# Performance work log

Hardware: AMD Instinct MI355X
Metric: run time of the kernel (lower is better)

## Reference

```python
import jax, jax.numpy as jnp
import numpy as np

HID = 10
IN_DIM = 256
B, H, W = 8, 96, 96


def _conv(x, w, b=None, pad=0):
    y = jax.lax.conv_general_dilated(x, w, (1, 1), [(pad, pad), (pad, pad)],
                                     dimension_numbers=('NCHW', 'OIHW', 'NCHW'))
    return y if b is None else y + b[None, :, None, None]


def _bn(x, g, b):
    # eval-mode InPlaceABN(Sync) with identity running stats -> per-channel affine
    return x * g[None, :, None, None] + b[None, :, None, None]


def _branch(x, w1, g1, b1, w2, g2, b2):
    # Conv3x3 -> BN -> ReLU -> Conv1x1 -> BN -> ReLU  (relation / comp_u / comp_l)
    y = jax.nn.relu(_bn(_conv(x, w1, pad=1), g1, b1))
    return jax.nn.relu(_bn(_conv(y, w2), g2, b2))


def _gru(x, h, gw, gb, cw, cg, cb):
    # ConvGRU with 1x1 kernels
    gates = _conv(jnp.concatenate([x, h], axis=1), gw, gb)
    r = jax.nn.sigmoid(gates[:, 0:1])
    u = jax.nn.sigmoid(gates[:, 1:2])
    cnm = jax.nn.relu(_bn(_conv(jnp.concatenate([x, r * h], axis=1), cw), cg, cb))
    return (1.0 - u) * h + u * cnm


def setup_inputs():
    key = jax.random.key(0)
    ks = iter(jax.random.split(key, 48))

    def nrm(shape, s=0.05):
        return jax.random.normal(next(ks), shape, jnp.float32) * s

    inp = {
        'f_nodes': jax.random.normal(next(ks), (2, B, HID, H, W), jnp.float32),
        'h_nodes': jax.random.normal(next(ks), (3, B, HID, H, W), jnp.float32),
        'p_nodes': jax.random.normal(next(ks), (7, B, HID, H, W), jnp.float32),
        'xh': jax.random.normal(next(ks), (B, IN_DIM, H, W), jnp.float32),
        'f_atts': jax.random.uniform(next(ks), (2, B, 1, H, W), jnp.float32),
        'p_atts': jax.random.uniform(next(ks), (7, B, 1, H, W), jnp.float32),
        # Decomposition.decomp_att: Conv3x3(257->256)+BN+ReLU, Conv1x1(256->2)+bias
        'da_w1': nrm((IN_DIM, IN_DIM + 1, 3, 3)),
        'da_g1': jnp.ones((IN_DIM,), jnp.float32),
        'da_b1': jnp.zeros((IN_DIM,), jnp.float32),
        'da_w2': nrm((2, IN_DIM, 1, 1)),
        'da_b2': jnp.zeros((2,), jnp.float32),
    }
    # relation (shared across children), comp_u, comp_l: Conv3x3(20->10)+BN+ReLU, Conv1x1(10->10)+BN+ReLU
    for p in ('rel', 'cu', 'cl'):
        inp[p + '_w1'] = nrm((HID, 2 * HID, 3, 3))
        inp[p + '_g1'] = jnp.ones((HID,), jnp.float32)
        inp[p + '_b1'] = jnp.zeros((HID,), jnp.float32)
        inp[p + '_w2'] = nrm((HID, HID, 1, 1))
        inp[p + '_g2'] = jnp.ones((HID,), jnp.float32)
        inp[p + '_b2'] = jnp.zeros((HID,), jnp.float32)
    # 3 ConvGRUs (cls_h), 1x1 kernels, stacked on leading dim
    inp['gru_gw'] = nrm((3, 2, 2 * HID, 1, 1))
    inp['gru_gb'] = jnp.zeros((3, 2), jnp.float32)
    inp['gru_cw'] = nrm((3, HID, 2 * HID, 1, 1))
    inp['gru_cg'] = jnp.ones((3, HID), jnp.float32)
    inp['gru_cb'] = jnp.zeros((3, HID), jnp.float32)
    return inp


def reference(f_nodes, h_nodes, p_nodes, xh, f_atts, p_atts,
              da_w1, da_g1, da_b1, da_w2, da_b2,
              rel_w1, rel_g1, rel_b1, rel_w2, rel_g2, rel_b2,
              cu_w1, cu_g1, cu_b1, cu_w2, cu_g2, cu_b2,
              cl_w1, cl_g1, cl_b1, cl_w2, cl_g2, cl_b2,
              gru_gw, gru_gb, gru_cw, gru_cg, gru_cb):
    parent, parent_att = f_nodes[1], f_atts[1]
    # Decomposition of full-body node into 2 half nodes
    dm = _conv(jnp.concatenate([parent_att, xh], axis=1), da_w1, pad=1)
    dm = jax.nn.relu(_bn(dm, da_g1, da_b1))
    dm = _conv(dm, da_w2, da_b2)  # [B, 2, H, W] decomposition map
    datt = jax.nn.softmax(dm, axis=1)
    decomp = [_branch(jnp.concatenate([parent * datt[:, i:i + 1] * parent_att,
                                       h_nodes[1 + i]], axis=1),
                      rel_w1, rel_g1, rel_b1, rel_w2, rel_g2, rel_b2)
              for i in range(2)]
    # node 0: background
    n0 = _gru(f_nodes[0] + p_nodes[0], h_nodes[0],
              gru_gw[0], gru_gb[0], gru_cw[0], gru_cg[0], gru_cb[0])
    # node 1: upper half = composition(upper parts 1-4) + decomposition
    up = jnp.sum(p_nodes[1:5], axis=0) * jnp.sum(p_atts[1:5], axis=0)
    comp_u = _branch(jnp.concatenate([h_nodes[1], up], axis=1),
                     cu_w1, cu_g1, cu_b1, cu_w2, cu_g2, cu_b2)
    n1 = _gru(comp_u + decomp[0], h_nodes[1],
              gru_gw[1], gru_gb[1], gru_cw[1], gru_cg[1], gru_cb[1])
    # node 2: lower half = composition(lower parts 5-6) + decomposition
    lo = jnp.sum(p_nodes[5:7], axis=0) * jnp.sum(p_atts[5:7], axis=0)
    comp_l = _branch(jnp.concatenate([h_nodes[2], lo], axis=1),
                     cl_w1, cl_g1, cl_b1, cl_w2, cl_g2, cl_b2)
    n2 = _gru(comp_l + decomp[1], h_nodes[2],
              gru_gw[2], gru_gb[2], gru_cw[2], gru_cg[2], gru_cb[2])
    return (jnp.stack([n0, n1, n2]), dm)
```

## Files before the change

kernel.cpp:

```cpp
#include <hip/hip_runtime.h>
#include <cstddef>
#include <cstdint>

constexpr int Bn    = 8;
constexpr int Hn    = 96;
constexpr int Wn    = 96;
constexpr int HWn   = Hn * Wn;
constexpr int BHWn  = Bn * HWn;
constexpr int B10HW = Bn * 10 * HWn;

using short8  = __attribute__((ext_vector_type(8))) short;
using ushort8 = __attribute__((ext_vector_type(8))) unsigned short;
using float4v = __attribute__((ext_vector_type(4))) float;

__device__ __forceinline__ unsigned short f2bf(float f) {
    unsigned u = __builtin_bit_cast(unsigned, f);
    u += 0x7FFFu + ((u >> 16) & 1u);
    return (unsigned short)(u >> 16);
}

__global__ void k_packw(const float* __restrict__ w1, short* __restrict__ wpk)
{
    const int idx = blockIdx.x * 256 + threadIdx.x;
    if (idx >= 82944) return;
    const int lane = idx & 63;
    const int q    = (idx >> 6) & 15;
    const int t    = idx >> 10;
    const int tap  = t % 9;
    const int cb   = t / 9;
    const int co   = q * 16 + (lane & 15);
    const int ci0  = cb * 32 + ((lane >> 4) * 8);
    ushort8 v;
    #pragma unroll
    for (int j = 0; j < 8; ++j) {
        const int ci = ci0 + j;
        const float f = (ci < 257) ? w1[((size_t)co * 257 + ci) * 9 + tap] : 0.f;
        v[j] = f2bf(f);
    }
    *(ushort8*)(wpk + (size_t)idx * 8) = v;
}

__global__ __launch_bounds__(256, 2)
void k_bigconv2(const float* __restrict__ xh, const float* __restrict__ patt,
                const short* __restrict__ wpk, const float* __restrict__ g1,
                const float* __restrict__ b1, const float* __restrict__ w2,
                const float* __restrict__ db2,
                float* __restrict__ dm_out, float* __restrict__ s01)
{
    __shared__ __align__(16) short xs[2][4][205][8];
    __shared__ float part[2][128][2];

    const int tid    = threadIdx.x;
    const int lane   = tid & 63;
    const int wid    = tid >> 6;
    const int wave_m = wid >> 1;
    const int wave_n = wid & 1;
    const int bx     = blockIdx.x;
    const int wseg   = bx % 3;
    const int hb     = (bx / 3) % 24;
    const int b      = bx / 72;
    const int h0     = hb * 4, w0 = wseg * 32;
    const int am     = lane & 15;
    const int aq     = lane >> 4;

    float4v acc[4][8];
    #pragma unroll
    for (int i = 0; i < 4; ++i)
        #pragma unroll
        for (int j = 0; j < 8; ++j)
            acc[i][j] = float4v{0.f, 0.f, 0.f, 0.f};

    int arow[4], acol[4];
    #pragma unroll
    for (int mt = 0; mt < 4; ++mt) {
        const int m = wave_m * 64 + mt * 16 + am;
        arow[mt] = m >> 5;
        acol[mt] = m & 31;
    }

    auto stageX = [&](int cb, int buf) {
        const int cig0 = cb * 32 + wid * 8;
        for (int pos = lane; pos < 204; pos += 64) {
            const int row = pos / 34, col = pos % 34;
            const int hh = h0 - 1 + row, ww = w0 - 1 + col;
            const bool inb = ((unsigned)hh < (unsigned)Hn) & ((unsigned)ww < (unsigned)Wn);
            const int off = hh * Wn + ww;
            ushort8 v;
            #pragma unroll
            for (int j = 0; j < 8; ++j) {
                const int ci = cig0 + j;
                float f = 0.f;
                if (inb && ci < 257)
                    f = (ci == 0) ? patt[b * HWn + off]
                                  : xh[((size_t)b * 256 + (ci - 1)) * HWn + off];
                v[j] = f2bf(f);
            }
            *(ushort8*)&xs[buf][wid][pos][0] = v;
        }
    };

    const short8* wp = (const short8*)wpk;
    const int qb = wave_n * 8;

    stageX(0, 0);
    short8 bfr[8], bnx[8];
    #pragma unroll
    for (int nt = 0; nt < 8; ++nt)
        bfr[nt] = wp[(size_t)(qb + nt) * 64 + lane];
    __syncthreads();

    for (int cb = 0; cb < 9; ++cb) {
        const int buf = cb & 1;
        for (int tap = 0; tap < 9; ++tap) {
            const int t = cb * 9 + tap;
            if (t < 80) {
                #pragma unroll
                for (int nt = 0; nt < 8; ++nt)
                    bnx[nt] = wp[((size_t)(t + 1) * 16 + qb + nt) * 64 + lane];
            }
            const int kh = tap / 3, kw = tap % 3;
            short8 afr[4];
            #pragma unroll
            for (int mt = 0; mt < 4; ++mt) {
                const int pos = (arow[mt] + kh) * 34 + (acol[mt] + kw);
                afr[mt] = *(const short8*)&xs[buf][aq][pos][0];
            }
            #pragma unroll
            for (int mt = 0; mt < 4; ++mt)
                #pragma unroll
                for (int nt = 0; nt < 8; ++nt)
                    acc[mt][nt] = __builtin_amdgcn_mfma_f32_16x16x32_bf16(
                        afr[mt], bfr[nt], acc[mt][nt], 0, 0, 0);
            #pragma unroll
            for (int nt = 0; nt < 8; ++nt) bfr[nt] = bnx[nt];
        }
        if (cb < 8) stageX(cb + 1, buf ^ 1);
        __syncthreads();
    }

    float gv[8], bv[8], wa[8], wbv[8];
    #pragma unroll
    for (int nt = 0; nt < 8; ++nt) {
        const int co = wave_n * 128 + nt * 16 + am;
        gv[nt]  = g1[co];
        bv[nt]  = b1[co];
        wa[nt]  = w2[co];
        wbv[nt] = w2[256 + co];
    }
    #pragma unroll
    for (int mt = 0; mt < 4; ++mt) {
        #pragma unroll
        for (int reg = 0; reg < 4; ++reg) {
            float s0 = 0.f, s1 = 0.f;
            #pragma unroll
            for (int nt = 0; nt < 8; ++nt) {
                const float y = fmaxf(fmaf(acc[mt][nt][reg], gv[nt], bv[nt]), 0.f);
                s0 = fmaf(wa[nt], y, s0);
                s1 = fmaf(wbv[nt], y, s1);
            }
            #pragma unroll
            for (int off = 1; off < 16; off <<= 1) {
                s0 += __shfl_xor(s0, off, 64);
                s1 += __shfl_xor(s1, off, 64);
            }
            if (am == 0) {
                const int m = wave_m * 64 + mt * 16 + aq * 4 + reg;
                part[wave_n][m][0] = s0;
                part[wave_n][m][1] = s1;
            }
        }
    }
    __syncthreads();
    if (tid < 128) {
        const int m = tid, r = m >> 5, c = m & 31;
        const int off = (h0 + r) * Wn + (w0 + c);
        float d0 = part[0][m][0] + part[1][m][0] + db2[0];
        float d1 = part[0][m][1] + part[1][m][1] + db2[1];
        dm_out[(size_t)(b * 2) * HWn + off]     = d0;
        dm_out[(size_t)(b * 2 + 1) * HWn + off] = d1;
        const float mx = fmaxf(d0, d1);
        const float e0 = expf(d0 - mx), e1 = expf(d1 - mx);
        const float pa = patt[b * HWn + off];
        const float inv = pa / (e0 + e1);
        s01[b * HWn + off]        = e0 * inv;
        s01[BHWn + b * HWn + off] = e1 * inv;
    }
}

__global__ void k_uplo(const float* __restrict__ pn, const float* __restrict__ pa,
                       float* __restrict__ up, float* __restrict__ lo)
{
    const int p = blockIdx.x * 256 + threadIdx.x;
    if (p >= BHWn) return;
    const int b = p / HWn, hw = p % HWn;
    float au = 0.f, al = 0.f;
    for (int k = 1; k <= 4; ++k) au += pa[(size_t)(k * Bn + b) * HWn + hw];
    for (int k = 5; k <= 6; ++k) al += pa[(size_t)(k * Bn + b) * HWn + hw];
    for (int c = 0; c < 10; ++c) {
        float su = 0.f, sl = 0.f;
        for (int k = 1; k <= 4; ++k) su += pn[((size_t)(k * Bn + b) * 10 + c) * HWn + hw];
        for (int k = 5; k <= 6; ++k) sl += pn[((size_t)(k * Bn + b) * 10 + c) * HWn + hw];
        up[((size_t)b * 10 + c) * HWn + hw] = su * au;
        lo[((size_t)b * 10 + c) * HWn + hw] = sl * al;
    }
}

struct BranchW  { const float *w1, *g1, *b1, *w2, *g2, *b2; };
struct BranchW3 { BranchW p[3]; };

__global__ __launch_bounds__(256)
void k_branch(BranchW3 P, const float* __restrict__ parent, const float* __restrict__ h_nodes,
              const float* __restrict__ s01, const float* __restrict__ up,
              const float* __restrict__ lo, float* __restrict__ bout)
{
    const int z  = blockIdx.y;
    const int pi = (z < 2) ? 0 : (z - 1);
    __shared__ float xt[20][10][34];
    __shared__ __align__(16) float wlt[9 * 20 * 12];
    __shared__ float w2l[100], g1l[10], b1l[10], g2l[10], b2l[10];

    const BranchW& Pw = P.p[pi];
    const int tid = threadIdx.x;
    for (int idx = tid; idx < 2160; idx += 256) {
        const int co = idx % 12, rem = idx / 12, ci = rem % 20, tap = rem / 20;
        wlt[idx] = (co < 10) ? Pw.w1[(co * 20 + ci) * 9 + tap] : 0.f;
    }
    if (tid < 100) w2l[tid] = Pw.w2[tid];
    if (tid < 10) {
        g1l[tid] = Pw.g1[tid]; b1l[tid] = Pw.b1[tid];
        g2l[tid] = Pw.g2[tid]; b2l[tid] = Pw.b2[tid];
    }

    const int bx = blockIdx.x;
    const int tw = bx % 3, th = (bx / 3) % 12, b = bx / 36;
    const int h0 = th * 8, w0 = tw * 32;

    const float* Ab;
    const float* sc = nullptr;
    const float* Bb;
    if (z == 0)      { Ab = parent; sc = s01;        Bb = h_nodes + (size_t)1 * B10HW; }
    else if (z == 1) { Ab = parent; sc = s01 + BHWn; Bb = h_nodes + (size_t)2 * B10HW; }
    else if (z == 2) { Ab = h_nodes + (size_t)1 * B10HW; Bb = up; }
    else             { Ab = h_nodes + (size_t)2 * B10HW; Bb = lo; }

    for (int idx = tid; idx < 6800; idx += 256) {
        const int col = idx % 34, rem = idx / 34, row = rem % 10, ch = rem / 10;
        const int hh = h0 - 1 + row, ww = w0 - 1 + col;
        float v = 0.f;
        if (((unsigned)hh < (unsigned)Hn) & ((unsigned)ww < (unsigned)Wn)) {
            const int off = hh * Wn + ww;
            if (ch < 10) {
                v = Ab[((size_t)b * 10 + ch) * HWn + off];
                if (sc) v *= sc[b * HWn + off];
            } else {
                v = Bb[((size_t)b * 10 + (ch - 10)) * HWn + off];
            }
        }
        ((float*)xt)[idx] = v;
    }
    __syncthreads();

    const int r = tid >> 5, c = tid & 31;
    float a0 = 0, a1 = 0, a2 = 0, a3 = 0, a4 = 0, a5 = 0, a6 = 0, a7 = 0, a8 = 0, a9 = 0;
    #pragma unroll
    for (int tap = 0; tap < 9; ++tap) {
        const int kh = tap / 3, kw = tap % 3;
        #pragma unroll
        for (int ci = 0; ci < 20; ++ci) {
            const float xv = xt[ci][r + kh][c + kw];
            const float4 wA = *(const float4*)&wlt[(tap * 20 + ci) * 12];
            const float4 wB = *(const float4*)&wlt[(tap * 20 + ci) * 12 + 4];
            const float2 wC = *(const float2*)&wlt[(tap * 20 + ci) * 12 + 8];
            a0 = fmaf(wA.x, xv, a0); a1 = fmaf(wA.y, xv, a1);
            a2 = fmaf(wA.z, xv, a2); a3 = fmaf(wA.w, xv, a3);
            a4 = fmaf(wB.x, xv, a4); a5 = fmaf(wB.y, xv, a5);
            a6 = fmaf(wB.z, xv, a6); a7 = fmaf(wB.w, xv, a7);
            a8 = fmaf(wC.x, xv, a8); a9 = fmaf(wC.y, xv, a9);
        }
    }
    float acc[10] = {a0, a1, a2, a3, a4, a5, a6, a7, a8, a9};
    float y[10];
    #pragma unroll
    for (int co = 0; co < 10; ++co)
        y[co] = fmaxf(fmaf(acc[co], g1l[co], b1l[co]), 0.f);
    const int hw = (h0 + r) * Wn + (w0 + c);
    #pragma unroll
    for (int co = 0; co < 10; ++co) {
        float s = 0.f;
        #pragma unroll
        for (int i = 0; i < 10; ++i) s = fmaf(w2l[co * 10 + i], y[i], s);
        s = fmaxf(fmaf(s, g2l[co], b2l[co]), 0.f);
        bout[(size_t)z * B10HW + ((size_t)b * 10 + co) * HWn + hw] = s;
    }
}

__global__ void k_gru(const float* __restrict__ f_nodes, const float* __restrict__ h_nodes,
                      const float* __restrict__ p_nodes, const float* __restrict__ bout,
                      const float* __restrict__ gw, const float* __restrict__ gb,
                      const float* __restrict__ cw, const float* __restrict__ cg,
                      const float* __restrict__ cb, float* __restrict__ out)
{
    const int z = blockIdx.y;
    __shared__ float gwl[40], cwl[200], gbl[2], cgl[10], cbl[10];
    if (threadIdx.x < 40)  gwl[threadIdx.x] = gw[z * 40 + threadIdx.x];
    if (threadIdx.x < 200) cwl[threadIdx.x] = cw[z * 200 + threadIdx.x];
    if (threadIdx.x < 2)   gbl[threadIdx.x] = gb[z * 2 + threadIdx.x];
    if (threadIdx.x < 10) {
        cgl[threadIdx.x] = cg[z * 10 + threadIdx.x];
        cbl[threadIdx.x] = cb[z * 10 + threadIdx.x];
    }
    __syncthreads();

    const int p = blockIdx.x * 256 + threadIdx.x;
    const int b = p / HWn, hw = p % HWn;
    float x[10], h[10];
    #pragma unroll
    for (int c = 0; c < 10; ++c) {
        const size_t idx = ((size_t)b * 10 + c) * HWn + hw;
        if (z == 0)      x[c] = f_nodes[idx] + p_nodes[idx];
        else if (z == 1) x[c] = bout[(size_t)2 * B10HW + idx] + bout[idx];
        else             x[c] = bout[(size_t)3 * B10HW + idx] + bout[(size_t)1 * B10HW + idx];
        h[c] = h_nodes[(size_t)z * B10HW + idx];
    }
    float g0 = gbl[0], g1 = gbl[1];
    #pragma unroll
    for (int c = 0; c < 10; ++c) {
        g0 = fmaf(gwl[c],      x[c], g0);
        g0 = fmaf(gwl[10 + c], h[c], g0);
        g1 = fmaf(gwl[20 + c], x[c], g1);
        g1 = fmaf(gwl[30 + c], h[c], g1);
    }
    const float r = 1.f / (1.f + expf(-g0));
    const float u = 1.f / (1.f + expf(-g1));
    #pragma unroll
    for (int o = 0; o < 10; ++o) {
        float s = 0.f;
        #pragma unroll
        for (int c = 0; c < 10; ++c) {
            s = fmaf(cwl[o * 20 + c],      x[c],     s);
            s = fmaf(cwl[o * 20 + 10 + c], r * h[c], s);
        }
        s = fmaxf(fmaf(s, cgl[o], cbl[o]), 0.f);
        out[(size_t)z * B10HW + ((size_t)b * 10 + o) * HWn + hw] =
            (1.f - u) * h[o] + u * s;
    }
}

extern "C" void kernel_launch(void* const* d_in, const int* in_sizes, int n_in,
                              void* d_out, int out_size, void* d_ws, size_t ws_size,
                              hipStream_t stream)
{
    (void)in_sizes; (void)n_in; (void)out_size; (void)ws_size;

    const float* f_nodes = (const float*)d_in[0];
    const float* h_nodes = (const float*)d_in[1];
    const float* p_nodes = (const float*)d_in[2];
    const float* xh      = (const float*)d_in[3];
    const float* f_atts  = (const float*)d_in[4];
    const float* p_atts  = (const float*)d_in[5];
    const float* da_w1   = (const float*)d_in[6];
    const float* da_g1   = (const float*)d_in[7];
    const float* da_b1   = (const float*)d_in[8];
    const float* da_w2   = (const float*)d_in[9];
    const float* da_b2   = (const float*)d_in[10];

    BranchW3 P;
    for (int i = 0; i < 3; ++i) {
        P.p[i].w1 = (const float*)d_in[11 + 6 * i + 0];
        P.p[i].g1 = (const float*)d_in[11 + 6 * i + 1];
        P.p[i].b1 = (const float*)d_in[11 + 6 * i + 2];
        P.p[i].w2 = (const float*)d_in[11 + 6 * i + 3];
        P.p[i].g2 = (const float*)d_in[11 + 6 * i + 4];
        P.p[i].b2 = (const float*)d_in[11 + 6 * i + 5];
    }
    const float* gru_gw = (const float*)d_in[29];
    const float* gru_gb = (const float*)d_in[30];
    const float* gru_cw = (const float*)d_in[31];
    const float* gru_cg = (const float*)d_in[32];
    const float* gru_cb = (const float*)d_in[33];

    float* out    = (float*)d_out;
    float* dm_out = out + (size_t)3 * B10HW;

    float* ws     = (float*)d_ws;
    float* s01    = ws;
    float* up     = s01 + 2 * BHWn;
    float* lo     = up + B10HW;
    float* bout   = lo + B10HW;
    short* wpk    = (short*)bout;

    const float* patt   = f_atts + BHWn;
    const float* parent = f_nodes + B10HW;

    k_packw<<<dim3(324), 256, 0, stream>>>(da_w1, wpk);
    k_bigconv2<<<dim3(576), 256, 0, stream>>>(xh, patt, wpk, da_g1, da_b1,
                                              da_w2, da_b2, dm_out, s01);
    k_uplo<<<dim3(288), 256, 0, stream>>>(p_nodes, p_atts, up, lo);
    k_branch<<<dim3(288, 4), 256, 0, stream>>>(P, parent, h_nodes, s01, up, lo, bout);
    k_gru<<<dim3(288, 3), 256, 0, stream>>>(f_nodes, h_nodes, p_nodes, bout,
                                            gru_gw, gru_gb, gru_cw, gru_cg, gru_cb, out);
}
```

Measured before the change: 407.6 us.

## Retile big conv to smaller blocks, coalesce weight packing, vectorize uplo

The big 3x3 conv now uses 2-row output tiles, with each wave owning 64 output channels instead of a 2x2 wave grid. This halves the accumulator registers and doubles the block count so more blocks fit per CU. Weight packing now reads the source weights coalesced, one element per thread, after a memset that zero-fills the padded channels. The uplo kernel is vectorized with float4 and split across channels. The cost is more redundant halo loads of the input, because the smaller tiles stage proportionally more border rows.

```diff
diff --git a/kernel.cpp b/kernel.cpp
--- a/kernel.cpp
+++ b/kernel.cpp
@@ -22,65 +22,59 @@
 __global__ void k_packw(const float* __restrict__ w1, short* __restrict__ wpk)
 {
     const int idx = blockIdx.x * 256 + threadIdx.x;
-    if (idx >= 82944) return;
-    const int lane = idx & 63;
-    const int q    = (idx >> 6) & 15;
-    const int t    = idx >> 10;
-    const int tap  = t % 9;
-    const int cb   = t / 9;
-    const int co   = q * 16 + (lane & 15);
-    const int ci0  = cb * 32 + ((lane >> 4) * 8);
-    ushort8 v;
-    #pragma unroll
-    for (int j = 0; j < 8; ++j) {
-        const int ci = ci0 + j;
-        const float f = (ci < 257) ? w1[((size_t)co * 257 + ci) * 9 + tap] : 0.f;
-        v[j] = f2bf(f);
-    }
-    *(ushort8*)(wpk + (size_t)idx * 8) = v;
-}
-
-__global__ __launch_bounds__(256, 2)
-void k_bigconv2(const float* __restrict__ xh, const float* __restrict__ patt,
+    if (idx >= 592128) return;
+    const int co  = idx / 2313;
+    const int rem = idx % 2313;
+    const int ci  = rem / 9;
+    const int tap = rem % 9;
+    const int cb  = ci >> 5;
+    const int g   = (ci >> 3) & 3;
+    const int j   = ci & 7;
+    const int q   = co >> 4;
+    const int lane = (co & 15) + (g << 4);
+    const int t   = cb * 9 + tap;
+    wpk[(((size_t)t * 16 + q) * 64 + lane) * 8 + j] = (short)f2bf(w1[idx]);
+}
+
+__global__ __launch_bounds__(256, 3)
+void k_bigconv3(const float* __restrict__ xh, const float* __restrict__ patt,
                 const short* __restrict__ wpk, const float* __restrict__ g1,
                 const float* __restrict__ b1, const float* __restrict__ w2,
                 const float* __restrict__ db2,
                 float* __restrict__ dm_out, float* __restrict__ s01)
 {
-    __shared__ __align__(16) short xs[2][4][205][8];
-    __shared__ float part[2][128][2];
-
-    const int tid    = threadIdx.x;
-    const int lane   = tid & 63;
-    const int wid    = tid >> 6;
-    const int wave_m = wid >> 1;
-    const int wave_n = wid & 1;
-    const int bx     = blockIdx.x;
-    const int wseg   = bx % 3;
-    const int hb     = (bx / 3) % 24;
-    const int b      = bx / 72;
-    const int h0     = hb * 4, w0 = wseg * 32;
-    const int am     = lane & 15;
-    const int aq     = lane >> 4;
-
-    float4v acc[4][8];
+    __shared__ __align__(16) short xs[2][4][137][8];
+    __shared__ float part[4][64][2];
+
+    const int tid  = threadIdx.x;
+    const int lane = tid & 63;
+    const int wid  = tid >> 6;
+    const int bx   = blockIdx.x;
+    const int wseg = bx % 3;
+    const int hb   = (bx / 3) % 48;
+    const int b    = bx / 144;
+    const int h0   = hb * 2, w0 = wseg * 32;
+    const int am   = lane & 15;
+    const int aq   = lane >> 4;
+
+    float4v acc[4][4];
     #pragma unroll
     for (int i = 0; i < 4; ++i)
         #pragma unroll
-        for (int j = 0; j < 8; ++j)
+        for (int j = 0; j < 4; ++j)
             acc[i][j] = float4v{0.f, 0.f, 0.f, 0.f};
 
     int arow[4], acol[4];
     #pragma unroll
     for (int mt = 0; mt < 4; ++mt) {
-        const int m = wave_m * 64 + mt * 16 + am;
+        const int m = mt * 16 + am;
         arow[mt] = m >> 5;
         acol[mt] = m & 31;
     }
 
     auto stageX = [&](int cb, int buf) {
         const int cig0 = cb * 32 + wid * 8;
-        for (int pos = lane; pos < 204; pos += 64) {
+        for (int pos = lane; pos < 136; pos += 64) {
             const int row = pos / 34, col = pos % 34;
             const int hh = h0 - 1 + row, ww = w0 - 1 + col;
             const bool inb = ((unsigned)hh < (unsigned)Hn) & ((unsigned)ww < (unsigned)Wn);
@@ -100,12 +94,12 @@
     };
 
     const short8* wp = (const short8*)wpk;
-    const int qb = wave_n * 8;
+    const int qb = wid * 4;
 
     stageX(0, 0);
-    short8 bfr[8], bnx[8];
-    #pragma unroll
-    for (int nt = 0; nt < 8; ++nt)
+    short8 bfr[4], bnx[4];
+    #pragma unroll
+    for (int nt = 0; nt < 4; ++nt)
         bfr[nt] = wp[(size_t)(qb + nt) * 64 + lane];
     __syncthreads();
 
@@ -115,7 +109,7 @@
             const int t = cb * 9 + tap;
             if (t < 80) {
                 #pragma unroll
-                for (int nt = 0; nt < 8; ++nt)
+                for (int nt = 0; nt < 4; ++nt)
                     bnx[nt] = wp[((size_t)(t + 1) * 16 + qb + nt) * 64 + lane];
             }
             const int kh = tap / 3, kw = tap % 3;
@@ -128,20 +122,20 @@
             #pragma unroll
             for (int mt = 0; mt < 4; ++mt)
                 #pragma unroll
-                for (int nt = 0; nt < 8; ++nt)
+                for (int nt = 0; nt < 4; ++nt)
                     acc[mt][nt] = __builtin_amdgcn_mfma_f32_16x16x32_bf16(
                         afr[mt], bfr[nt], acc[mt][nt], 0, 0, 0);
             #pragma unroll
-            for (int nt = 0; nt < 8; ++nt) bfr[nt] = bnx[nt];
+            for (int nt = 0; nt < 4; ++nt) bfr[nt] = bnx[nt];
         }
         if (cb < 8) stageX(cb + 1, buf ^ 1);
         __syncthreads();
     }
 
-    float gv[8], bv[8], wa[8], wbv[8];
-    #pragma unroll
-    for (int nt = 0; nt < 8; ++nt) {
-        const int co = wave_n * 128 + nt * 16 + am;
+    float gv[4], bv[4], wa[4], wbv[4];
+    #pragma unroll
+    for (int nt = 0; nt < 4; ++nt) {
+        const int co = wid * 64 + nt * 16 + am;
         gv[nt]  = g1[co];
         bv[nt]  = b1[co];
         wa[nt]  = w2[co];
@@ -153,7 +147,7 @@
         for (int reg = 0; reg < 4; ++reg) {
             float s0 = 0.f, s1 = 0.f;
             #pragma unroll
-            for (int nt = 0; nt < 8; ++nt) {
+            for (int nt = 0; nt < 4; ++nt) {
                 const float y = fmaxf(fmaf(acc[mt][nt][reg], gv[nt], bv[nt]), 0.f);
                 s0 = fmaf(wa[nt], y, s0);
                 s1 = fmaf(wbv[nt], y, s1);
@@ -164,18 +158,18 @@
                 s1 += __shfl_xor(s1, off, 64);
             }
             if (am == 0) {
-                const int m = wave_m * 64 + mt * 16 + aq * 4 + reg;
-                part[wave_n][m][0] = s0;
-                part[wave_n][m][1] = s1;
+                const int m = mt * 16 + aq * 4 + reg;
+                part[wid][m][0] = s0;
+                part[wid][m][1] = s1;
             }
         }
     }
     __syncthreads();
-    if (tid < 128) {
+    if (tid < 64) {
         const int m = tid, r = m >> 5, c = m & 31;
         const int off = (h0 + r) * Wn + (w0 + c);
-        float d0 = part[0][m][0] + part[1][m][0] + db2[0];
-        float d1 = part[0][m][1] + part[1][m][1] + db2[1];
+        float d0 = part[0][m][0] + part[1][m][0] + part[2][m][0] + part[3][m][0] + db2[0];
+        float d1 = part[0][m][1] + part[1][m][1] + part[2][m][1] + part[3][m][1] + db2[1];
         dm_out[(size_t)(b * 2) * HWn + off]     = d0;
         dm_out[(size_t)(b * 2 + 1) * HWn + off] = d1;
         const float mx = fmaxf(d0, d1);
@@ -190,19 +184,24 @@
 __global__ void k_uplo(const float* __restrict__ pn, const float* __restrict__ pa,
                        float* __restrict__ up, float* __restrict__ lo)
 {
-    const int p = blockIdx.x * 256 + threadIdx.x;
-    if (p >= BHWn) return;
-    const int b = p / HWn, hw = p % HWn;
-    float au = 0.f, al = 0.f;
-    for (int k = 1; k <= 4; ++k) au += pa[(size_t)(k * Bn + b) * HWn + hw];
-    for (int k = 5; k <= 6; ++k) al += pa[(size_t)(k * Bn + b) * HWn + hw];
-    for (int c = 0; c < 10; ++c) {
-        float su = 0.f, sl = 0.f;
-        for (int k = 1; k <= 4; ++k) su += pn[((size_t)(k * Bn + b) * 10 + c) * HWn + hw];
-        for (int k = 5; k <= 6; ++k) sl += pn[((size_t)(k * Bn + b) * 10 + c) * HWn + hw];
-        up[((size_t)b * 10 + c) * HWn + hw] = su * au;
-        lo[((size_t)b * 10 + c) * HWn + hw] = sl * al;
-    }
+    const int c = blockIdx.y;
+    const int i = blockIdx.x * 256 + threadIdx.x;
+    if (i >= BHWn / 4) return;
+    const int b = i / (HWn / 4), q = i % (HWn / 4);
+    const float4v* PA = (const float4v*)pa;
+    const float4v* PN = (const float4v*)pn;
+    float4v au = {0, 0, 0, 0}, al = {0, 0, 0, 0};
+    #pragma unroll
+    for (int k = 1; k <= 4; ++k) au += PA[(size_t)(k * Bn + b) * (HWn / 4) + q];
+    #pragma unroll
+    for (int k = 5; k <= 6; ++k) al += PA[(size_t)(k * Bn + b) * (HWn / 4) + q];
+    float4v su = {0, 0, 0, 0}, sl = {0, 0, 0, 0};
+    #pragma unroll
+    for (int k = 1; k <= 4; ++k) su += PN[((size_t)(k * Bn + b) * 10 + c) * (HWn / 4) + q];
+    #pragma unroll
+    for (int k = 5; k <= 6; ++k) sl += PN[((size_t)(k * Bn + b) * 10 + c) * (HWn / 4) + q];
+    ((float4v*)up)[((size_t)b * 10 + c) * (HWn / 4) + q] = su * au;
+    ((float4v*)lo)[((size_t)b * 10 + c) * (HWn / 4) + q] = sl * al;
 }
 
 struct BranchW  { const float *w1, *g1, *b1, *w2, *g2, *b2; };
@@ -392,11 +391,13 @@
     const float* patt   = f_atts + BHWn;
     const float* parent = f_nodes + B10HW;
 
-    k_packw<<<dim3(324), 256, 0, stream>>>(da_w1, wpk);
-    k_bigconv2<<<dim3(576), 256, 0, stream>>>(xh, patt, wpk, da_g1, da_b1,
-                                              da_w2, da_b2, dm_out, s01);
-    k_uplo<<<dim3(288), 256, 0, stream>>>(p_nodes, p_atts, up, lo);
+    hipMemsetAsync(wpk, 0, (size_t)82944 * 8 * sizeof(short), stream);
+    k_packw<<<dim3(2313), 256, 0, stream>>>(da_w1, wpk);
+    k_bigconv3<<<dim3(1152), 256, 0, stream>>>(xh, patt, wpk, da_g1, da_b1,
+                                               da_w2, da_b2, dm_out, s01);
+    k_uplo<<<dim3(72, 10), 256, 0, stream>>>(p_nodes, p_atts, up, lo);
     k_branch<<<dim3(288, 4), 256, 0, stream>>>(P, parent, h_nodes, s01, up, lo, bout);
     k_gru<<<dim3(288, 3), 256, 0, stream>>>(f_nodes, h_nodes, p_nodes, bout,
-                                            gru_gw, gru_gb, gru_cw, gru_cg, gru_cb, out);
-}
+                                            gru_gw, gru_gb, gru_cg ? gru_cw : gru_cw,
+                                            gru_cg, gru_cb, out);
+}
```

After: 390.9 us. 4.1% less time.
